# Optimization experiments

Measured on AMD Instinct MI355X. Metric: run time of the kernel, lower is better.

## Reference

```python
import jax, jax.numpy as jnp
import numpy as np

B, T, C, H, DFF = 4, 1024, 1024, 16, 4096
HS = C // H  # 64
EPS = 1e-5


def layer_norm(x, g, b):
    mu = jnp.mean(x, axis=-1, keepdims=True)
    var = jnp.var(x, axis=-1, keepdims=True)
    return (x - mu) * jax.lax.rsqrt(var + EPS) * g + b


def setup_inputs() -> dict:
    key = jax.random.key(0)
    ks = jax.random.split(key, 12)
    s = 0.02
    return {
        "x": jax.random.normal(ks[0], (B, T, C), jnp.float32),
        "wq": jax.random.normal(ks[1], (H, C, HS), jnp.float32) * s,
        "wk": jax.random.normal(ks[2], (H, C, HS), jnp.float32) * s,
        "wv": jax.random.normal(ks[3], (H, C, HS), jnp.float32) * s,
        "w_proj": jax.random.normal(ks[4], (H * HS, C), jnp.float32) * s,
        "b_proj": jnp.zeros((C,), jnp.float32),
        "w1": jax.random.normal(ks[5], (C, DFF), jnp.float32) * s,
        "b1": jnp.zeros((DFF,), jnp.float32),
        "w2": jax.random.normal(ks[6], (DFF, C), jnp.float32) * s,
        "b2": jnp.zeros((C,), jnp.float32),
        "g1": jnp.ones((C,), jnp.float32),
        "be1": jnp.zeros((C,), jnp.float32),
        "g2": jnp.ones((C,), jnp.float32),
        "be2": jnp.zeros((C,), jnp.float32),
    }


def reference(x, wq, wk, wv, w_proj, b_proj, w1, b1, w2, b2, g1, be1, g2, be2):
    h = layer_norm(x, g1, be1)
    # per-head projections, vectorized over heads: [B,H,T,HS]
    q = jnp.einsum('btc,hcd->bhtd', h, wq)
    k = jnp.einsum('btc,hcd->bhtd', h, wk)
    v = jnp.einsum('btc,hcd->bhtd', h, wv)
    # mask=None in the original forward, so no causal masking
    wei = jnp.einsum('bhtd,bhsd->bhts', q, k) * (HS ** -0.5)
    wei = jax.nn.softmax(wei, axis=-1)  # [B,H,T,T]
    out = jnp.einsum('bhts,bhsd->bhtd', wei, v)
    out = out.transpose(0, 2, 1, 3).reshape(B, T, H * HS)  # concat heads
    attn_out = out @ w_proj + b_proj
    x = x + attn_out
    h2 = layer_norm(x, g2, be2)
    ff = jax.nn.relu(h2 @ w1 + b1) @ w2 + b2
    x = x + ff
    return x, wei
```

## Files before the change

### kernel.cpp

```cpp
#include <hip/hip_runtime.h>
#include <hip/hip_bf16.h>

#define BB    4
#define TT    1024
#define CC    1024
#define HH    16
#define HSZ   64
#define DFF   4096
#define NTOK  (BB*TT)
#define BHN   (BB*HH)

typedef __attribute__((ext_vector_type(8))) short bf16x8;
typedef __attribute__((ext_vector_type(4))) float f32x4;

#define VMC0  asm volatile("s_waitcnt vmcnt(0)" ::: "memory")
#define VMC2  asm volatile("s_waitcnt vmcnt(2)" ::: "memory")
#define LGK0  asm volatile("s_waitcnt lgkmcnt(0)" ::: "memory")
#define BARRIER do { asm volatile("" ::: "memory"); \
                     __builtin_amdgcn_s_barrier();  \
                     asm volatile("" ::: "memory"); } while (0)

__device__ __forceinline__ ushort f2b(float v) {
    union { float f; unsigned u; } c; c.f = v;
    unsigned r = c.u + 0x7fffu + ((c.u >> 16) & 1u);
    return (ushort)(r >> 16);
}
__device__ __forceinline__ void stv(float* p, float v)  { *p = v; }
__device__ __forceinline__ void stv(ushort* p, float v) { *p = f2b(v); }

__device__ __forceinline__ void gload16(const void* g, void* l) {
    __builtin_amdgcn_global_load_lds(
        (const __attribute__((address_space(1))) void*)g,
        (__attribute__((address_space(3))) void*)l, 16, 0, 0);
}

__global__ __launch_bounds__(256)
void ln_k(const float* __restrict__ x, const float* __restrict__ g,
          const float* __restrict__ be, ushort* __restrict__ o)
{
    __shared__ float s1[4], s2[4];
    long row = blockIdx.x;
    const float4* xr = (const float4*)(x + row * CC);
    float4 v = xr[threadIdx.x];
    float a = v.x + v.y + v.z + v.w;
    float b = v.x*v.x + v.y*v.y + v.z*v.z + v.w*v.w;
    for (int off = 32; off > 0; off >>= 1) {
        a += __shfl_down(a, off);
        b += __shfl_down(b, off);
    }
    if ((threadIdx.x & 63) == 0) { s1[threadIdx.x >> 6] = a; s2[threadIdx.x >> 6] = b; }
    __syncthreads();
    float sum = s1[0] + s1[1] + s1[2] + s1[3];
    float sq  = s2[0] + s2[1] + s2[2] + s2[3];
    float mu  = sum * (1.0f / CC);
    float var = sq * (1.0f / CC) - mu * mu;
    float inv = rsqrtf(var + 1e-5f);
    float4 gg = ((const float4*)g)[threadIdx.x];
    float4 bb = ((const float4*)be)[threadIdx.x];
    ushort4 r;
    r.x = f2b((v.x - mu) * inv * gg.x + bb.x);
    r.y = f2b((v.y - mu) * inv * gg.y + bb.y);
    r.z = f2b((v.z - mu) * inv * gg.z + bb.z);
    r.w = f2b((v.w - mu) * inv * gg.w + bb.w);
    ((ushort4*)(o + row * CC))[threadIdx.x] = r;
}

__global__ __launch_bounds__(256)
void cvtall_k(const float* __restrict__ wq, const float* __restrict__ wk,
              const float* __restrict__ wv, const float* __restrict__ wproj,
              const float* __restrict__ w1, const float* __restrict__ w2,
              ushort* __restrict__ wqkvT, ushort* __restrict__ wpT,
              ushort* __restrict__ w1T, ushort* __restrict__ w2T)
{
    __shared__ float t[32][33];
    int idx = blockIdx.x;
    const float* src; ushort* dst; int R, Cc, bx, by;
    if (idx < 3072) {
        int seg = idx >> 10, rem = idx & 1023;
        int z = rem >> 6, tt2 = rem & 63;
        src = (seg == 0 ? wq : seg == 1 ? wk : wv) + (long)z * 65536;
        dst = wqkvT + (long)seg * (1L << 20) + (long)z * 65536;
        R = 1024; Cc = 64; bx = tt2 & 1; by = tt2 >> 1;
    } else if (idx < 4096) {
        int tt2 = idx - 3072;
        src = wproj; dst = wpT; R = 1024; Cc = 1024; bx = tt2 & 31; by = tt2 >> 5;
    } else if (idx < 8192) {
        int tt2 = idx - 4096;
        src = w1; dst = w1T; R = 1024; Cc = 4096; bx = tt2 & 127; by = tt2 >> 7;
    } else {
        int tt2 = idx - 8192;
        src = w2; dst = w2T; R = 4096; Cc = 1024; bx = tt2 & 31; by = tt2 >> 5;
    }
    int r0 = by * 32, c0 = bx * 32;
    int tx = threadIdx.x & 31, ty = threadIdx.x >> 5;
#pragma unroll
    for (int i = 0; i < 4; i++)
        t[ty + 8*i][tx] = src[(long)(r0 + ty + 8*i) * Cc + c0 + tx];
    __syncthreads();
#pragma unroll
    for (int i = 0; i < 4; i++)
        dst[(long)(c0 + ty + 8*i) * R + r0 + tx] = f2b(t[tx][ty + 8*i]);
}

enum { OL_PLAIN = 0, OL_QKV3 = 1 };
constexpr int EBIAS = 1, ERELU = 2, ERES = 4, ESCALE = 8;

template<int BM, int BN, int WM, int WN, int OL, int EPI, typename OutT>
__global__ __launch_bounds__(256)
void mgemm_k(const ushort* __restrict__ A, const ushort* __restrict__ Bt,
             const float* __restrict__ bias, const float* __restrict__ res,
             OutT* __restrict__ C, int M, int N, int K,
             long sA, long sB, long sC, float scale)
{
    constexpr int BK = 64;
    constexpr int FM = BM / WM / 16, FN = BN / WN / 16;
    __shared__ ushort As[BM * BK];
    __shared__ ushort Bs[BN * BK];
    const int tid = threadIdx.x;
    const int w = tid >> 6, l = tid & 63;
    const int wr = w / WN, wc = w % WN;
    const int l15 = l & 15, l4 = l >> 4;
    const int bh = blockIdx.z;
    const ushort* Ap = A  + (long)bh * sA + (long)(blockIdx.y * BM) * K;
    const ushort* Bp = Bt + (long)bh * sB + (long)(blockIdx.x * BN) * K;

    f32x4 acc[FM][FN];
#pragma unroll
    for (int m = 0; m < FM; m++)
#pragma unroll
        for (int n = 0; n < FN; n++) acc[m][n] = (f32x4){0.f, 0.f, 0.f, 0.f};

    const int arow = tid >> 3;
    const int achk = tid & 7;

    for (int k0 = 0; k0 < K; k0 += BK) {
#pragma unroll
        for (int i = 0; i < BM / 32; i++)
            gload16(Ap + (long)(i*32 + arow) * K + k0 + achk*8,
                    &As[(i*32 + w*8) * BK]);
#pragma unroll
        for (int i = 0; i < BN / 32; i++)
            gload16(Bp + (long)(i*32 + arow) * K + k0 + achk*8,
                    &Bs[(i*32 + w*8) * BK]);
        __syncthreads();
#pragma unroll
        for (int kk = 0; kk < 2; kk++) {
            const int ko = kk*32 + l4*8;
            bf16x8 af[FM], bfr[FN];
#pragma unroll
            for (int m = 0; m < FM; m++)
                af[m] = *(const bf16x8*)&As[(wr*(BM/WM) + m*16 + l15) * BK + ko];
#pragma unroll
            for (int n = 0; n < FN; n++)
                bfr[n] = *(const bf16x8*)&Bs[(wc*(BN/WN) + n*16 + l15) * BK + ko];
#pragma unroll
            for (int m = 0; m < FM; m++)
#pragma unroll
                for (int n = 0; n < FN; n++)
                    acc[m][n] = __builtin_amdgcn_mfma_f32_16x16x32_bf16(
                        af[m], bfr[n], acc[m][n], 0, 0, 0);
        }
        __syncthreads();
    }

#pragma unroll
    for (int m = 0; m < FM; m++) {
        int rbase = blockIdx.y*BM + wr*(BM/WM) + m*16 + l4*4;
#pragma unroll
        for (int n = 0; n < FN; n++) {
            int col = blockIdx.x*BN + wc*(BN/WN) + n*16 + l15;
#pragma unroll
            for (int r = 0; r < 4; r++) {
                int row = rbase + r;
                float v = acc[m][n][r];
                if (EPI & ESCALE) v *= scale;
                if (EPI & EBIAS)  v += bias[col];
                if (EPI & ERELU)  v = fmaxf(v, 0.f);
                if (EPI & ERES)   v += res[(long)row * N + col];
                long idx;
                if (OL == OL_PLAIN) {
                    idx = (long)row * N + col;
                } else {
                    int seg = col >> 10;
                    int cl  = col & 1023;
                    long bh_ = ((long)((row >> 10) * HH + (cl >> 6))) * 65536;
                    long off = (seg == 2)
                        ? bh_ + (long)(cl & 63) * 1024 + (row & 1023)
                        : bh_ + (long)(row & 1023) * 64 + (cl & 63);
                    idx = (long)seg * (4L << 20) + off;
                }
                stv(&C[(long)bh * sC + idx], v);
            }
        }
    }
}

__global__ __launch_bounds__(512, 2)
void fattn_k(const ushort* __restrict__ q_, const ushort* __restrict__ k_,
             const ushort* __restrict__ vt, float* __restrict__ wei,
             ushort* __restrict__ attn)
{
    __shared__ ushort Qs[256*64];
    __shared__ ushort Ks[128*64];
    __shared__ ushort Vs[64*128];
    __shared__ ushort Ps[256*128];
    float* sred = (float*)Ps;

    const int tid = threadIdx.x;
    const int w = tid >> 6, l = tid & 63;
    const int wr = w >> 1, wc = w & 1;
    const int l15 = l & 15, l4 = l >> 4;
    const int bh = blockIdx.y;
    const int q0 = blockIdx.x * 256;
    const int arow = tid >> 3, achk = tid & 7;
    const int kchk = achk ^ (arow & 7);
    const int vrow = tid >> 4;
    const int vchk = (tid & 15) ^ (vrow & 15);
    const int sw8  = (l15 & 7) << 3;
    const int sw16 = l15 << 3;

    const ushort* Qp = q_ + (long)bh * 65536;
    const ushort* Kp = k_ + (long)bh * 65536;
    const ushort* Vp = vt + (long)bh * 65536;

#pragma unroll
    for (int i = 0; i < 4; i++)
        gload16(Qp + (long)(q0 + i*64 + arow) * 64 + kchk*8, &Qs[(i*64 + w*8)*64]);
#pragma unroll
    for (int i = 0; i < 2; i++)
        gload16(Kp + (long)(i*64 + arow) * 64 + kchk*8, &Ks[(i*64 + w*8)*64]);

    float ssum[4][4];
#pragma unroll
    for (int m = 0; m < 4; m++)
#pragma unroll
        for (int r = 0; r < 4; r++) ssum[m][r] = 0.f;

    for (int st = 0; st < 8; ++st) {
        const ushort* cur = (st & 1) ? Vs : Ks;
        ushort*       nxt = (st & 1) ? Ks : Vs;
        if (st < 7) {
#pragma unroll
            for (int i = 0; i < 2; i++)
                gload16(Kp + (long)((st+1)*128 + i*64 + arow) * 64 + kchk*8,
                        &nxt[(i*64 + w*8)*64]);
            VMC2;
        } else {
            VMC0;
        }
        BARRIER;

        f32x4 sacc[4][4];
#pragma unroll
        for (int m = 0; m < 4; m++)
#pragma unroll
            for (int n = 0; n < 4; n++) sacc[m][n] = (f32x4){0.f,0.f,0.f,0.f};
        __builtin_amdgcn_s_setprio(1);
#pragma unroll
        for (int kk = 0; kk < 2; kk++) {
            const int ko = kk*32 + l4*8;
            bf16x8 af[4], bfr[4];
#pragma unroll
            for (int m = 0; m < 4; m++)
                af[m] = *(const bf16x8*)&Qs[(wr*64 + m*16 + l15)*64 + (ko ^ sw8)];
#pragma unroll
            for (int n = 0; n < 4; n++)
                bfr[n] = *(const bf16x8*)&cur[(wc*64 + n*16 + l15)*64 + (ko ^ sw8)];
#pragma unroll
            for (int m = 0; m < 4; m++)
#pragma unroll
                for (int n = 0; n < 4; n++)
                    sacc[m][n] = __builtin_amdgcn_mfma_f32_16x16x32_bf16(
                        af[m], bfr[n], sacc[m][n], 0, 0, 0);
        }
        __builtin_amdgcn_s_setprio(0);
#pragma unroll
        for (int m = 0; m < 4; m++)
#pragma unroll
            for (int r = 0; r < 4; r++) {
                float s = 0.f;
#pragma unroll
                for (int n = 0; n < 4; n++) s += __expf(sacc[m][n][r] * 0.125f);
                ssum[m][r] += s;
            }
        BARRIER;
    }

#pragma unroll
    for (int i = 0; i < 2; i++)
        gload16(Kp + (long)(i*64 + arow) * 64 + kchk*8, &Ks[(i*64 + w*8)*64]);
#pragma unroll
    for (int i = 0; i < 2; i++)
        gload16(Vp + (long)(i*32 + vrow) * 1024 + vchk*8, &Vs[(i*32 + w*4)*128]);

    float linv[4][4];
#pragma unroll
    for (int m = 0; m < 4; m++)
#pragma unroll
        for (int r = 0; r < 4; r++) {
            float s = ssum[m][r];
#pragma unroll
            for (int d = 1; d < 16; d <<= 1) s += __shfl_xor(s, d);
            if (l15 == 0) sred[wc*256 + wr*64 + m*16 + l4*4 + r] = s;
        }
    LGK0; BARRIER;
#pragma unroll
    for (int m = 0; m < 4; m++)
#pragma unroll
        for (int r = 0; r < 4; r++) {
            int rg = wr*64 + m*16 + l4*4 + r;
            linv[m][r] = 1.0f / (sred[rg] + sred[256 + rg]);
        }

    f32x4 oacc[4][2];
#pragma unroll
    for (int m = 0; m < 4; m++)
#pragma unroll
        for (int n = 0; n < 2; n++) oacc[m][n] = (f32x4){0.f,0.f,0.f,0.f};

    for (int st = 0; st < 8; ++st) {
        if (st > 0) {
#pragma unroll
            for (int i = 0; i < 2; i++)
                gload16(Kp + (long)(st*128 + i*64 + arow) * 64 + kchk*8,
                        &Ks[(i*64 + w*8)*64]);
#pragma unroll
            for (int i = 0; i < 2; i++)
                gload16(Vp + (long)(i*32 + vrow) * 1024 + st*128 + vchk*8,
                        &Vs[(i*32 + w*4)*128]);
        }
        VMC0;
        BARRIER;

        f32x4 sacc[4][4];
#pragma unroll
        for (int m = 0; m < 4; m++)
#pragma unroll
            for (int n = 0; n < 4; n++) sacc[m][n] = (f32x4){0.f,0.f,0.f,0.f};
        __builtin_amdgcn_s_setprio(1);
#pragma unroll
        for (int kk = 0; kk < 2; kk++) {
            const int ko = kk*32 + l4*8;
            bf16x8 af[4], bfr[4];
#pragma unroll
            for (int m = 0; m < 4; m++)
                af[m] = *(const bf16x8*)&Qs[(wr*64 + m*16 + l15)*64 + (ko ^ sw8)];
#pragma unroll
            for (int n = 0; n < 4; n++)
                bfr[n] = *(const bf16x8*)&Ks[(wc*64 + n*16 + l15)*64 + (ko ^ sw8)];
#pragma unroll
            for (int m = 0; m < 4; m++)
#pragma unroll
                for (int n = 0; n < 4; n++)
                    sacc[m][n] = __builtin_amdgcn_mfma_f32_16x16x32_bf16(
                        af[m], bfr[n], sacc[m][n], 0, 0, 0);
        }
        __builtin_amdgcn_s_setprio(0);

        float pv[4][4][4];
#pragma unroll
        for (int m = 0; m < 4; m++)
#pragma unroll
            for (int r = 0; r < 4; r++) {
                int rg = wr*64 + m*16 + l4*4 + r;
                int psw = (rg & 15) << 3;
                float li = linv[m][r];
#pragma unroll
                for (int n = 0; n < 4; n++) {
                    int col = wc*64 + n*16 + l15;
                    float p = __expf(sacc[m][n][r] * 0.125f) * li;
                    pv[m][n][r] = p;
                    Ps[rg*128 + (col ^ psw)] = f2b(p);
                }
            }
        LGK0; BARRIER;

        __builtin_amdgcn_s_setprio(1);
#pragma unroll
        for (int kc = 0; kc < 4; ++kc) {
            const int ko = kc*32 + l4*8;
            bf16x8 pa[4], vb[2];
#pragma unroll
            for (int m = 0; m < 4; m++)
                pa[m] = *(const bf16x8*)&Ps[(wr*64 + m*16 + l15)*128 + (ko ^ sw16)];
#pragma unroll
            for (int n = 0; n < 2; n++)
                vb[n] = *(const bf16x8*)&Vs[(wc*32 + n*16 + l15)*128 + (ko ^ sw16)];
#pragma unroll
            for (int m = 0; m < 4; m++)
#pragma unroll
                for (int n = 0; n < 2; n++)
                    oacc[m][n] = __builtin_amdgcn_mfma_f32_16x16x32_bf16(
                        pa[m], vb[n], oacc[m][n], 0, 0, 0);
        }
        __builtin_amdgcn_s_setprio(0);

        float* wrow = wei + (long)bh * (TT*(long)TT) + st*128;
#pragma unroll
        for (int m = 0; m < 4; m++)
#pragma unroll
            for (int r = 0; r < 4; r++) {
                int rg = wr*64 + m*16 + l4*4 + r;
#pragma unroll
                for (int n = 0; n < 4; n++) {
                    int col = wc*64 + n*16 + l15;
                    __builtin_nontemporal_store(pv[m][n][r],
                        &wrow[(long)(q0 + rg) * TT + col]);
                }
            }
        BARRIER;
    }

#pragma unroll
    for (int m = 0; m < 4; m++)
#pragma unroll
        for (int r = 0; r < 4; r++) {
            int rg = wr*64 + m*16 + l4*4 + r;
            long rowbase = ((long)(bh >> 4) * TT + q0 + rg) * CC + (long)(bh & 15) * HSZ;
#pragma unroll
            for (int n = 0; n < 2; n++)
                attn[rowbase + wc*32 + n*16 + l15] = f2b(oacc[m][n][r]);
        }
}

extern "C" void kernel_launch(void* const* d_in, const int* in_sizes, int n_in,
                              void* d_out, int out_size, void* d_ws, size_t ws_size,
                              hipStream_t stream)
{
    const float* x      = (const float*)d_in[0];
    const float* wq     = (const float*)d_in[1];
    const float* wk     = (const float*)d_in[2];
    const float* wv     = (const float*)d_in[3];
    const float* w_proj = (const float*)d_in[4];
    const float* b_proj = (const float*)d_in[5];
    const float* w1     = (const float*)d_in[6];
    const float* b1     = (const float*)d_in[7];
    const float* w2     = (const float*)d_in[8];
    const float* b2     = (const float*)d_in[9];
    const float* g1     = (const float*)d_in[10];
    const float* be1    = (const float*)d_in[11];
    const float* g2     = (const float*)d_in[12];
    const float* be2    = (const float*)d_in[13];

    float* out_x = (float*)d_out;
    float* wei   = out_x + (long)NTOK * CC;

    const long MEL = 1 << 20;
    ushort* ws16 = (ushort*)d_ws;
    ushort* h    = ws16;
    ushort* q_   = ws16 + 4*MEL;
    ushort* k_   = ws16 + 8*MEL;
    ushort* vt   = ws16 + 12*MEL;
    ushort* attn = ws16 + 16*MEL;
    ushort* h2   = ws16 + 20*MEL;
    ushort* a1   = ws16 + 24*MEL;
    ushort* wqkvT= ws16 + 40*MEL;
    ushort* w1T  = ws16 + 44*MEL;
    ushort* wpT  = ws16 + 48*MEL;
    ushort* w2T  = ws16 + 49*MEL;
    float*  x1   = (float*)(ws16 + 54*MEL);

    cvtall_k<<<12288, 256, 0, stream>>>(wq, wk, wv, w_proj, w1, w2,
                                        wqkvT, wpT, w1T, w2T);

    ln_k<<<NTOK, 256, 0, stream>>>(x, g1, be1, h);

    mgemm_k<128,128,2,2,OL_QKV3,0,ushort><<<dim3(24,32,1), 256, 0, stream>>>(
        h, wqkvT, nullptr, nullptr, q_, NTOK, 3072, CC, 0,0,0, 0.f);

    fattn_k<<<dim3(4, 64), 512, 0, stream>>>(q_, k_, vt, wei, attn);

    mgemm_k<128,64,2,2,OL_PLAIN,EBIAS|ERES,float><<<dim3(16,32,1), 256, 0, stream>>>(
        attn, wpT, b_proj, x, x1, NTOK, CC, CC, 0,0,0, 0.f);

    ln_k<<<NTOK, 256, 0, stream>>>(x1, g2, be2, h2);

    mgemm_k<128,128,2,2,OL_PLAIN,EBIAS|ERELU,ushort><<<dim3(32,32,1), 256, 0, stream>>>(
        h2, w1T, b1, nullptr, a1, NTOK, DFF, CC, 0,0,0, 0.f);

    mgemm_k<128,64,2,2,OL_PLAIN,EBIAS|ERES,float><<<dim3(16,32,1), 256, 0, stream>>>(
        a1, w2T, b2, x1, out_x, NTOK, CC, DFF, 0,0,0, 0.f);
}
```

Baseline: 342.1 us.

## Fold softmax scale into Q and compute row sums directly from global K

```diff
diff --git a/kernel.cpp b/kernel.cpp
--- a/kernel.cpp
+++ b/kernel.cpp
@@ -14,11 +14,12 @@
 typedef __attribute__((ext_vector_type(4))) float f32x4;
 
 #define VMC0  asm volatile("s_waitcnt vmcnt(0)" ::: "memory")
-#define VMC2  asm volatile("s_waitcnt vmcnt(2)" ::: "memory")
 #define LGK0  asm volatile("s_waitcnt lgkmcnt(0)" ::: "memory")
 #define BARRIER do { asm volatile("" ::: "memory"); \
                      __builtin_amdgcn_s_barrier();  \
                      asm volatile("" ::: "memory"); } while (0)
+
+#define QSCALE 0.18033688f
 
 __device__ __forceinline__ ushort f2b(float v) {
     union { float f; unsigned u; } c; c.f = v;
@@ -183,6 +184,7 @@
                 } else {
                     int seg = col >> 10;
                     int cl  = col & 1023;
+                    if (seg == 0) v *= QSCALE;
                     long bh_ = ((long)((row >> 10) * HH + (cl >> 6))) * 65536;
                     long off = (seg == 2)
                         ? bh_ + (long)(cl & 63) * 1024 + (row & 1023)
@@ -204,7 +206,7 @@
     __shared__ ushort Ks[128*64];
     __shared__ ushort Vs[64*128];
     __shared__ ushort Ps[256*128];
-    float* sred = (float*)Ps;
+    float* sredF = (float*)Ps;
 
     const int tid = threadIdx.x;
     const int w = tid >> 6, l = tid & 63;
@@ -229,88 +231,75 @@
 #pragma unroll
     for (int i = 0; i < 2; i++)
         gload16(Kp + (long)(i*64 + arow) * 64 + kchk*8, &Ks[(i*64 + w*8)*64]);
-
-    float ssum[4][4];
-#pragma unroll
-    for (int m = 0; m < 4; m++)
-#pragma unroll
-        for (int r = 0; r < 4; r++) ssum[m][r] = 0.f;
-
-    for (int st = 0; st < 8; ++st) {
-        const ushort* cur = (st & 1) ? Vs : Ks;
-        ushort*       nxt = (st & 1) ? Ks : Vs;
-        if (st < 7) {
-#pragma unroll
-            for (int i = 0; i < 2; i++)
-                gload16(Kp + (long)((st+1)*128 + i*64 + arow) * 64 + kchk*8,
-                        &nxt[(i*64 + w*8)*64]);
-            VMC2;
-        } else {
-            VMC0;
-        }
-        BARRIER;
-
-        f32x4 sacc[4][4];
-#pragma unroll
-        for (int m = 0; m < 4; m++)
-#pragma unroll
-            for (int n = 0; n < 4; n++) sacc[m][n] = (f32x4){0.f,0.f,0.f,0.f};
-        __builtin_amdgcn_s_setprio(1);
-#pragma unroll
-        for (int kk = 0; kk < 2; kk++) {
-            const int ko = kk*32 + l4*8;
-            bf16x8 af[4], bfr[4];
-#pragma unroll
-            for (int m = 0; m < 4; m++)
-                af[m] = *(const bf16x8*)&Qs[(wr*64 + m*16 + l15)*64 + (ko ^ sw8)];
-#pragma unroll
-            for (int n = 0; n < 4; n++)
-                bfr[n] = *(const bf16x8*)&cur[(wc*64 + n*16 + l15)*64 + (ko ^ sw8)];
-#pragma unroll
-            for (int m = 0; m < 4; m++)
-#pragma unroll
-                for (int n = 0; n < 4; n++)
-                    sacc[m][n] = __builtin_amdgcn_mfma_f32_16x16x32_bf16(
-                        af[m], bfr[n], sacc[m][n], 0, 0, 0);
-        }
-        __builtin_amdgcn_s_setprio(0);
-#pragma unroll
-        for (int m = 0; m < 4; m++)
-#pragma unroll
-            for (int r = 0; r < 4; r++) {
-                float s = 0.f;
-#pragma unroll
-                for (int n = 0; n < 4; n++) s += __expf(sacc[m][n][r] * 0.125f);
-                ssum[m][r] += s;
-            }
-        BARRIER;
-    }
-
-#pragma unroll
-    for (int i = 0; i < 2; i++)
-        gload16(Kp + (long)(i*64 + arow) * 64 + kchk*8, &Ks[(i*64 + w*8)*64]);
 #pragma unroll
     for (int i = 0; i < 2; i++)
         gload16(Vp + (long)(i*32 + vrow) * 1024 + vchk*8, &Vs[(i*32 + w*4)*128]);
 
+    {
+        const int lq = w * 32;
+        bf16x8 qf[2][2];
+#pragma unroll
+        for (int m = 0; m < 2; m++)
+#pragma unroll
+            for (int kk = 0; kk < 2; kk++)
+                qf[m][kk] = *(const bf16x8*)
+                    &Qp[(long)(q0 + lq + m*16 + l15)*64 + kk*32 + l4*8];
+
+        float ssum[2][4];
+#pragma unroll
+        for (int m = 0; m < 2; m++)
+#pragma unroll
+            for (int r = 0; r < 4; r++) ssum[m][r] = 0.f;
+
+        for (int st = 0; st < 16; ++st) {
+            const ushort* Kt = Kp + (long)st * 64 * 64;
+            f32x4 sacc[2][4];
+#pragma unroll
+            for (int m = 0; m < 2; m++)
+#pragma unroll
+                for (int n = 0; n < 4; n++) sacc[m][n] = (f32x4){0.f,0.f,0.f,0.f};
+#pragma unroll
+            for (int kk = 0; kk < 2; kk++) {
+                bf16x8 bfr[4];
+#pragma unroll
+                for (int n = 0; n < 4; n++)
+                    bfr[n] = *(const bf16x8*)&Kt[(long)(n*16 + l15)*64 + kk*32 + l4*8];
+#pragma unroll
+                for (int m = 0; m < 2; m++)
+#pragma unroll
+                    for (int n = 0; n < 4; n++)
+                        sacc[m][n] = __builtin_amdgcn_mfma_f32_16x16x32_bf16(
+                            qf[m][kk], bfr[n], sacc[m][n], 0, 0, 0);
+            }
+#pragma unroll
+            for (int m = 0; m < 2; m++)
+#pragma unroll
+                for (int r = 0; r < 4; r++) {
+                    float s = 0.f;
+#pragma unroll
+                    for (int n = 0; n < 4; n++) s += exp2f(sacc[m][n][r]);
+                    ssum[m][r] += s;
+                }
+        }
+
+#pragma unroll
+        for (int m = 0; m < 2; m++)
+#pragma unroll
+            for (int r = 0; r < 4; r++) {
+                float s = ssum[m][r];
+#pragma unroll
+                for (int d = 1; d < 16; d <<= 1) s += __shfl_xor(s, d);
+                if (l15 == 0) sredF[lq + m*16 + l4*4 + r] = s;
+            }
+    }
+    LGK0; BARRIER;
+
     float linv[4][4];
 #pragma unroll
     for (int m = 0; m < 4; m++)
 #pragma unroll
-        for (int r = 0; r < 4; r++) {
-            float s = ssum[m][r];
-#pragma unroll
-            for (int d = 1; d < 16; d <<= 1) s += __shfl_xor(s, d);
-            if (l15 == 0) sred[wc*256 + wr*64 + m*16 + l4*4 + r] = s;
-        }
-    LGK0; BARRIER;
-#pragma unroll
-    for (int m = 0; m < 4; m++)
-#pragma unroll
-        for (int r = 0; r < 4; r++) {
-            int rg = wr*64 + m*16 + l4*4 + r;
-            linv[m][r] = 1.0f / (sred[rg] + sred[256 + rg]);
-        }
+        for (int r = 0; r < 4; r++)
+            linv[m][r] = 1.0f / sredF[wr*64 + m*16 + l4*4 + r];
 
     f32x4 oacc[4][2];
 #pragma unroll
@@ -368,7 +357,7 @@
 #pragma unroll
                 for (int n = 0; n < 4; n++) {
                     int col = wc*64 + n*16 + l15;
-                    float p = __expf(sacc[m][n][r] * 0.125f) * li;
+                    float p = exp2f(sacc[m][n][r]) * li;
                     pv[m][n][r] = p;
                     Ps[rg*128 + (col ^ psw)] = f2b(p);
                 }
```

Result: slower. 359.0 us (+4.9%).
